# Kernel tuning notes

Hardware: AMD Instinct MI355X
Metric: run time of the kernel (lower is better)

The kernel has to match this reference:

```python
import jax, jax.numpy as jnp
import numpy as np

N, E = 100000, 1600000          # nodes, edges
H, DH = 8, 256                  # heads, dim_hidden
D = DH // H                     # dim per head
NEG_SLOPE = 0.2                 # GAT leaky_relu slope
BETA = 0.5


def setup_inputs() -> dict:
    key = jax.random.key(0)
    ks = jax.random.split(key, 10)
    s = 1.0 / np.sqrt(DH)
    return {
        "x": jax.random.normal(ks[0], (N, DH), jnp.float32),
        "edge_index": jax.random.randint(ks[1], (2, E), 0, N, jnp.int32),
        "edge_attr": jax.random.uniform(ks[2], (E,), jnp.float32),
        # GAT params (no bias, add_self_loops=False)
        "Wg": jax.random.normal(ks[3], (DH, DH), jnp.float32) * s,
        "att_src": jax.random.normal(ks[4], (H, D), jnp.float32) * s,
        "att_dst": jax.random.normal(ks[5], (H, D), jnp.float32) * s,
        # h_lin
        "Wh": jax.random.normal(ks[6], (DH, DH), jnp.float32) * s,
        "bh": jnp.zeros((DH,), jnp.float32),
        # lin
        "Wl": jax.random.normal(ks[7], (DH, DH), jnp.float32) * s,
        "bl": jnp.zeros((DH,), jnp.float32),
        # LayerNorm
        "ln_g": jnp.ones((DH,), jnp.float32),
        "ln_b": jnp.zeros((DH,), jnp.float32),
        # beta gate (beta>=0 -> constant vector)
        "b_param": jnp.full((DH,), BETA, jnp.float32),
    }


def _layer_norm(v, g, b, eps=1e-5):
    mu = jnp.mean(v, axis=-1, keepdims=True)
    var = jnp.var(v, axis=-1, keepdims=True)
    return (v - mu) * jax.lax.rsqrt(var + eps) * g + b


def _weighted_gat(x, edge_index, edge_attr, Wg, att_src, att_dst):
    # GATConv with per-edge weights folded into the softmax numerator.
    xs = (x @ Wg).reshape(N, H, D)                       # [N,H,D]
    a_src = jnp.einsum("nhd,hd->nh", xs, att_src)        # [N,H]
    a_dst = jnp.einsum("nhd,hd->nh", xs, att_dst)
    src, dst = edge_index[0], edge_index[1]
    e = jax.nn.leaky_relu(a_src[src] + a_dst[dst], NEG_SLOPE)   # [E,H]
    m = jax.ops.segment_max(e, dst, num_segments=N)             # [N,H]
    m = jnp.where(jnp.isfinite(m), m, 0.0)                      # isolated nodes
    p = jnp.exp(e - m[dst]) * edge_attr[:, None]                # weighted exp
    denom = jax.ops.segment_sum(p, dst, num_segments=N)         # [N,H]
    alpha = p / (denom[dst] + 1e-16)                            # [E,H]
    msg = alpha[:, :, None] * xs[src]                           # [E,H,D]
    out = jax.ops.segment_sum(msg, dst, num_segments=N)         # [N,H,D]
    return out.reshape(N, DH)


def reference(x, edge_index, edge_attr, Wg, att_src, att_dst, Wh, bh, Wl, bl, ln_g, ln_b, b_param):
    x_in = x
    h = jax.nn.relu(x @ Wh + bh)
    xg = _weighted_gat(x, edge_index, edge_attr, Wg, att_src, att_dst) + (x @ Wl + bl)
    xg = jax.nn.relu(xg)                                  # dropout p=0 (eval)
    beta = b_param[None, :]
    out = (1.0 - beta) * _layer_norm(h * xg, ln_g, ln_b) + beta * xg
    return out + x_in                                     # residual=True
```

## Files before the change

### kernel.cpp

```cpp
#include <hip/hip_runtime.h>

typedef __attribute__((ext_vector_type(4))) float f32x4;
typedef __attribute__((ext_vector_type(8))) __bf16 bf16x8;

__device__ __forceinline__ unsigned short f2bf(float f) {
    return __builtin_bit_cast(unsigned short, (__bf16)f);
}
__device__ __forceinline__ float bf2f(unsigned short u) {
    return __builtin_bit_cast(float, (unsigned)u << 16);
}

__device__ __forceinline__ void gload16(const void* g, void* l) {
    __builtin_amdgcn_global_load_lds(
        (const __attribute__((address_space(1))) void*)g,
        (__attribute__((address_space(3))) void*)l, 16, 0, 0);
}

__global__ __launch_bounds__(256) void k_prep(
    const float* __restrict__ x, unsigned short* __restrict__ xb, long total, long totalPad,
    const float* __restrict__ Wg, const float* __restrict__ Wh, const float* __restrict__ Wl,
    unsigned short* __restrict__ wt,
    const int* __restrict__ dst, int E, int* __restrict__ deg,
    int nCvt, int nHist) {
    const int b = blockIdx.x;
    const int tid = threadIdx.x;
    if (b < nCvt) {
        long i = ((long)b * 256 + tid) * 4;
        if (i >= totalPad) return;
        if (i < total) {
            float4 v = *(const float4*)(x + i);
            ushort4 u;
            u.x = f2bf(v.x); u.y = f2bf(v.y); u.z = f2bf(v.z); u.w = f2bf(v.w);
            *(ushort4*)(xb + i) = u;
        } else {
            ushort4 u = {0, 0, 0, 0};
            *(ushort4*)(xb + i) = u;
        }
    } else if (b < nCvt + 768) {
        int t = (b - nCvt) * 256 + tid;
        int nn = t >> 8, k = t & 255;
        const float* W = (nn < 256) ? Wg : (nn < 512) ? Wh : Wl;
        wt[t] = f2bf(W[k * 256 + (nn & 255)]);
    } else {
        int bb = b - nCvt - 768;
        for (int e = bb * 256 + tid; e < E; e += nHist * 256)
            atomicAdd(&deg[dst[e]], 1);
    }
}

__global__ __launch_bounds__(256, 4) void k_gemm(
    const unsigned short* __restrict__ A,
    const unsigned short* __restrict__ BT,
    unsigned short* __restrict__ xs, unsigned short* __restrict__ hb,
    unsigned short* __restrict__ xlb,
    const float* __restrict__ bh, const float* __restrict__ bl, int M, int nwg) {
    __shared__ char Asm[32768];
    const int bid = blockIdx.x;
    const int xcd = bid & 7, idx = bid >> 3;
    const int q = nwg >> 3, r = nwg & 7;
    const int tm = (xcd < r ? xcd * (q + 1) : r * (q + 1) + (xcd - r) * q) + idx;

    const int tid = threadIdx.x;
    const int lane = tid & 63;
    const int wave = tid >> 6;
    const int wn = wave * 32;
    const int fr = lane & 15;
    const int ko = (lane >> 4) * 8;

#pragma unroll
    for (int s = 0; s < 8; ++s) {
        const int c = s * 256 + tid;
        const int rr = c & 15;
        const int kc = (c >> 4) & 31;
        const int m16 = c >> 9;
        const unsigned short* g = A + (size_t)(tm * 64 + m16 * 16 + rr) * 256 + kc * 8;
        gload16(g, Asm + (size_t)c * 16);
    }
    __syncthreads();

    const char* Ab = Asm + lane * 16;

    for (int tn = 0; tn < 6; ++tn) {
        f32x4 acc[4][2] = {};
        const unsigned short* Bg = BT + (size_t)(tn * 128 + wn + fr) * 256 + ko;
#pragma unroll
        for (int ks = 0; ks < 8; ++ks) {
            bf16x8 bfr[2], af[4];
#pragma unroll
            for (int j = 0; j < 2; ++j)
                bfr[j] = *(const bf16x8*)(Bg + (size_t)j * 16 * 256 + ks * 32);
#pragma unroll
            for (int i = 0; i < 4; ++i)
                af[i] = *(const bf16x8*)(Ab + i * 8192 + ks * 1024);
#pragma unroll
            for (int i = 0; i < 4; ++i)
#pragma unroll
                for (int j = 0; j < 2; ++j)
                    acc[i][j] = __builtin_amdgcn_mfma_f32_16x16x32_bf16(af[i], bfr[j], acc[i][j], 0, 0, 0);
        }
        const int ob = tn >> 1;
        unsigned short* obuf = (ob == 0) ? xs : (ob == 1) ? hb : xlb;
        const float* bias = (ob == 1) ? bh : bl;
        const int rbase = tm * 64 + (lane >> 4) * 4;
#pragma unroll
        for (int i = 0; i < 4; ++i) {
#pragma unroll
            for (int j = 0; j < 2; ++j) {
                const int c0 = (tn & 1) * 128 + wn + j * 16 + fr;
                float bv = (ob == 0) ? 0.f : bias[c0];
#pragma unroll
                for (int q2 = 0; q2 < 4; ++q2) {
                    const int rg = rbase + i * 16 + q2;
                    if (rg < M) {
                        float v = acc[i][j][q2] + bv;
                        if (ob == 1) v = v > 0.f ? v : 0.f;
                        obuf[(size_t)rg * 256 + c0] = f2bf(v);
                    }
                }
            }
        }
    }
}

__global__ __launch_bounds__(256) void k_attn(const unsigned short* __restrict__ xs,
                                              const float* __restrict__ att_src,
                                              const float* __restrict__ att_dst,
                                              float* __restrict__ a_src,
                                              float* __restrict__ a_dst, int N) {
    int t = blockIdx.x * 256 + threadIdx.x;
    int n = t >> 3, hh = t & 7;
    if (n >= N) return;
    const ushort4* xp = (const ushort4*)(xs + (size_t)n * 256 + hh * 32);
    const float4* sp = (const float4*)(att_src + hh * 32);
    const float4* dp = (const float4*)(att_dst + hh * 32);
    float sa = 0.f, sd = 0.f;
#pragma unroll
    for (int q = 0; q < 8; ++q) {
        ushort4 u = xp[q];
        float4 s = sp[q], d = dp[q];
        float v0 = bf2f(u.x), v1 = bf2f(u.y), v2 = bf2f(u.z), v3 = bf2f(u.w);
        sa += v0 * s.x + v1 * s.y + v2 * s.z + v3 * s.w;
        sd += v0 * d.x + v1 * d.y + v2 * d.z + v3 * d.w;
    }
    a_src[t] = sa;
    a_dst[t] = sd;
}

__global__ __launch_bounds__(256) void k_scan1(const int* __restrict__ deg, int* __restrict__ offs,
                                               int* __restrict__ bsum, int Npad) {
    __shared__ int s[256];
    int t = threadIdx.x;
    int i = blockIdx.x * 256 + t;
    int v = (i < Npad) ? ((deg[i] + 7) & ~7) : 0;
    s[t] = v;
    __syncthreads();
#pragma unroll
    for (int off = 1; off < 256; off <<= 1) {
        int x = (t >= off) ? s[t - off] : 0;
        __syncthreads();
        s[t] += x;
        __syncthreads();
    }
    offs[i] = s[t] - v;
    if (t == 255) bsum[blockIdx.x] = s[255];
}

__global__ __launch_bounds__(512) void k_scan2(int* __restrict__ bsum, int nb) {
    __shared__ int s[512];
    int t = threadIdx.x;
    int v = (t < nb) ? bsum[t] : 0;
    s[t] = v;
    __syncthreads();
#pragma unroll
    for (int off = 1; off < 512; off <<= 1) {
        int x = (t >= off) ? s[t - off] : 0;
        __syncthreads();
        s[t] += x;
        __syncthreads();
    }
    if (t < nb) bsum[t] = s[t] - v;
}

__global__ __launch_bounds__(256) void k_scan3(int* __restrict__ offs, const int* __restrict__ bsum,
                                               int* __restrict__ cursor) {
    int i = blockIdx.x * 256 + threadIdx.x;
    int o = offs[i] + bsum[blockIdx.x];
    offs[i] = o;
    cursor[i] = o;
}

__global__ void k_edge(const int* __restrict__ ei, const float* __restrict__ ea, int E,
                       const float* __restrict__ a_src, const float* __restrict__ a_dst,
                       int* __restrict__ cursor, int* __restrict__ srcArr,
                       unsigned short* __restrict__ pvArr) {
    for (int e = blockIdx.x * blockDim.x + threadIdx.x; e < E; e += gridDim.x * blockDim.x) {
        const int s = ei[e];
        const int d = ei[(size_t)E + e];
        const float w = ea[e];
        const int pos = atomicAdd(&cursor[d], 1);
        const float4* As = (const float4*)(a_src + (size_t)s * 8);
        const float4* Ad = (const float4*)(a_dst + (size_t)d * 8);
        float4 s0 = As[0], s1 = As[1], d0 = Ad[0], d1 = Ad[1];
        float a[8] = {s0.x + d0.x, s0.y + d0.y, s0.z + d0.z, s0.w + d0.w,
                      s1.x + d1.x, s1.y + d1.y, s1.z + d1.z, s1.w + d1.w};
        unsigned pk[4];
#pragma unroll
        for (int h = 0; h < 4; ++h) {
            float lo = a[2 * h], hi = a[2 * h + 1];
            lo = (lo > 0.f) ? lo : 0.2f * lo;
            hi = (hi > 0.f) ? hi : 0.2f * hi;
            unsigned short plo = f2bf(__expf(lo) * w);
            unsigned short phi = f2bf(__expf(hi) * w);
            pk[h] = (unsigned)plo | ((unsigned)phi << 16);
        }
        srcArr[pos] = s;
        uint4 v = {pk[0], pk[1], pk[2], pk[3]};
        *(uint4*)(pvArr + (size_t)pos * 8) = v;
    }
}

__global__ __launch_bounds__(256) void k_agg(
    const int* __restrict__ offs, const int* __restrict__ deg,
    const int* __restrict__ srcArr, const unsigned short* __restrict__ pvArr,
    const unsigned short* __restrict__ xs, const unsigned short* __restrict__ hb,
    const unsigned short* __restrict__ xlb,
    const unsigned short* __restrict__ xbf, const float* __restrict__ ln_g,
    const float* __restrict__ ln_b,
    const float* __restrict__ beta, float* __restrict__ out, int N) {
    const int wave = threadIdx.x >> 6, lane = threadIdx.x & 63;
    const int n = blockIdx.x * 4 + wave;
    if (n >= N) return;
    const int start = offs[n];
    const int dpad = (deg[n] + 7) & ~7;
    const int head = lane >> 3;
    const int eSub = lane & 7;

    f32x4 acc = {0.f, 0.f, 0.f, 0.f};
    float dsum = 0.f;

    const int* sp = srcArr + start;
    const unsigned short* pp = pvArr + (size_t)start * 8 + head;
    const char* xsb = (const char*)xs;
    const unsigned rowoff = (unsigned)lane * 8;

    for (int g = 0; g < dpad; g += 8) {
        const int sA = sp[g + eSub];
        ushort4 rows[8];
        float pvv[8];
#pragma unroll
        for (int e = 0; e < 8; ++e)
            rows[e] = *(const ushort4*)(xsb + (size_t)(unsigned)__shfl(sA, e) * 512 + rowoff);
#pragma unroll
        for (int e = 0; e < 8; ++e)
            pvv[e] = bf2f(pp[(size_t)(g + e) * 8]);
#pragma unroll
        for (int e = 0; e < 8; ++e) {
            const float p = pvv[e];
            dsum += p;
            acc[0] += p * bf2f(rows[e].x);
            acc[1] += p * bf2f(rows[e].y);
            acc[2] += p * bf2f(rows[e].z);
            acc[3] += p * bf2f(rows[e].w);
        }
    }
    const float inv = 1.f / (dsum + 1e-16f);

    const size_t base = (size_t)n * 256 + lane * 4;
    ushort4 xlu = *(const ushort4*)(xlb + base);
    ushort4 hu = *(const ushort4*)(hb + base);
    ushort4 xiu = *(const ushort4*)(xbf + base);
    f32x4 xg, t4;
    float s1 = 0.f, s2 = 0.f;
    const float xl0[4] = {bf2f(xlu.x), bf2f(xlu.y), bf2f(xlu.z), bf2f(xlu.w)};
    const float hv0[4] = {bf2f(hu.x), bf2f(hu.y), bf2f(hu.z), bf2f(hu.w)};
    const float xi0[4] = {bf2f(xiu.x), bf2f(xiu.y), bf2f(xiu.z), bf2f(xiu.w)};
#pragma unroll
    for (int q = 0; q < 4; ++q) {
        float gg = acc[q] * inv + xl0[q];
        gg = gg > 0.f ? gg : 0.f;
        xg[q] = gg;
        float t = hv0[q] * gg;
        t4[q] = t;
        s1 += t;
        s2 += t * t;
    }
#pragma unroll
    for (int off = 32; off; off >>= 1) {
        s1 += __shfl_xor(s1, off);
        s2 += __shfl_xor(s2, off);
    }
    const float mu = s1 * (1.f / 256.f);
    const float var = s2 * (1.f / 256.f) - mu * mu;
    const float rs = rsqrtf(var + 1e-5f);

    f32x4 g4 = *(const f32x4*)(ln_g + lane * 4);
    f32x4 b4 = *(const f32x4*)(ln_b + lane * 4);
    f32x4 be = *(const f32x4*)(beta + lane * 4);
    f32x4 o;
#pragma unroll
    for (int q = 0; q < 4; ++q) {
        float ln = (t4[q] - mu) * rs * g4[q] + b4[q];
        o[q] = (1.f - be[q]) * ln + be[q] * xg[q] + xi0[q];
    }
    *(f32x4*)(out + base) = o;
}

extern "C" void kernel_launch(void* const* d_in, const int* in_sizes, int n_in,
                              void* d_out, int out_size, void* d_ws, size_t ws_size,
                              hipStream_t stream) {
    const float* x = (const float*)d_in[0];
    const int* ei = (const int*)d_in[1];
    const float* ea = (const float*)d_in[2];
    const float* Wg = (const float*)d_in[3];
    const float* att_src = (const float*)d_in[4];
    const float* att_dst = (const float*)d_in[5];
    const float* Wh = (const float*)d_in[6];
    const float* bh = (const float*)d_in[7];
    const float* Wl = (const float*)d_in[8];
    const float* bl = (const float*)d_in[9];
    const float* ln_g = (const float*)d_in[10];
    const float* ln_b = (const float*)d_in[11];
    const float* beta = (const float*)d_in[12];
    float* out = (float*)d_out;

    const int DH = 256;
    const int N = in_sizes[0] / DH;
    const int E = in_sizes[2];
    const int Mpad = ((N + 127) / 128) * 128;
    const int Npad = ((N + 255) / 256) * 256;
    const int nscanb = Npad / 256;
    const int nwg = Mpad / 64;
    const int nCvt = Mpad / 4;
    const int nHist = 2048;
    const size_t Epad = (size_t)E + 8 * (size_t)N;

    char* w = (char*)d_ws;
    auto take = [&](size_t bytes) -> char* {
        char* p = w;
        w += (bytes + 255) & ~(size_t)255;
        return p;
    };
    unsigned short* xs = (unsigned short*)take((size_t)N * DH * 2);
    unsigned short* hb = (unsigned short*)take((size_t)N * DH * 2);
    unsigned short* xlb = (unsigned short*)take((size_t)N * DH * 2);
    float* a_src = (float*)take((size_t)N * 8 * 4);
    float* a_dst = (float*)take((size_t)N * 8 * 4);
    unsigned short* xbf = (unsigned short*)take((size_t)Mpad * DH * 2);
    unsigned short* wt = (unsigned short*)take((size_t)768 * 256 * 2);
    int* deg = (int*)take((size_t)Npad * 4);
    int* offs = (int*)take((size_t)Npad * 4);
    int* cursor = (int*)take((size_t)Npad * 4);
    int* bsum = (int*)take(512 * 4);
    int* srcArr = (int*)take(Epad * 4);
    unsigned short* pvArr = (unsigned short*)take(Epad * 8 * 2);

    hipMemsetAsync(deg, 0, (size_t)Npad * 4, stream);
    hipMemsetAsync(srcArr, 0, Epad * 4, stream);
    hipMemsetAsync(pvArr, 0, Epad * 8 * 2, stream);

    k_prep<<<nCvt + 768 + nHist, 256, 0, stream>>>(x, xbf, (long)N * DH, (long)Mpad * DH,
                                                   Wg, Wh, Wl, wt, ei + E, E, deg, nCvt, nHist);

    k_scan1<<<nscanb, 256, 0, stream>>>(deg, offs, bsum, Npad);
    k_scan2<<<1, 512, 0, stream>>>(bsum, nscanb);
    k_scan3<<<nscanb, 256, 0, stream>>>(offs, bsum, cursor);

    k_gemm<<<nwg, 256, 0, stream>>>(xbf, wt, xs, hb, xlb, bh, bl, N, nwg);

    k_attn<<<(N * 8 + 255) / 256, 256, 0, stream>>>(xs, att_src, att_dst, a_src, a_dst, N);

    k_edge<<<2048, 256, 0, stream>>>(ei, ea, E, a_src, a_dst, cursor, srcArr, pvArr);

    k_agg<<<(N + 3) / 4, 256, 0, stream>>>(offs, deg, srcArr, pvArr,
                                           xs, hb, xlb, xbf, ln_g, ln_b, beta, out, N);
}
```

Measured before the change: 700.3 us.

## Restructure GEMM to keep weight tile in LDS and stream pre-tiled activation blocks

The prep kernel now writes x in bf16 already in the MFMA tile-cell layout, and the three weight matrices pre-transposed into the same cell layout. The GEMM becomes a grid of (row-block × 12 column tiles of 64). Each workgroup loads its 64-column weight slice into LDS once, then loops over 16 consecutive 64-row A tiles with a 2×2 wave split. This replaces per-iteration global B reads and makes A loads fully contiguous. The residual in the aggregation kernel now reads the original fp32 x instead of the bf16 copy. In exchange, each A tile is now reloaded by 12 workgroups, and the A-tile reload is serialized behind barriers.

```diff
diff --git a/kernel.cpp b/kernel.cpp
--- a/kernel.cpp
+++ b/kernel.cpp
@@ -17,97 +17,116 @@
 }
 
 __global__ __launch_bounds__(256) void k_prep(
-    const float* __restrict__ x, unsigned short* __restrict__ xb, long total, long totalPad,
+    const float* __restrict__ x, unsigned short* __restrict__ xA, int N,
     const float* __restrict__ Wg, const float* __restrict__ Wh, const float* __restrict__ Wl,
-    unsigned short* __restrict__ wt,
+    unsigned short* __restrict__ wtc,
     const int* __restrict__ dst, int E, int* __restrict__ deg,
-    int nCvt, int nHist) {
+    int nACell, int nWtc, int nHist) {
     const int b = blockIdx.x;
     const int tid = threadIdx.x;
-    if (b < nCvt) {
-        long i = ((long)b * 256 + tid) * 4;
-        if (i >= totalPad) return;
-        if (i < total) {
-            float4 v = *(const float4*)(x + i);
-            ushort4 u;
-            u.x = f2bf(v.x); u.y = f2bf(v.y); u.z = f2bf(v.z); u.w = f2bf(v.w);
-            *(ushort4*)(xb + i) = u;
-        } else {
-            ushort4 u = {0, 0, 0, 0};
-            *(ushort4*)(xb + i) = u;
-        }
-    } else if (b < nCvt + 768) {
-        int t = (b - nCvt) * 256 + tid;
-        int nn = t >> 8, k = t & 255;
-        const float* W = (nn < 256) ? Wg : (nn < 512) ? Wh : Wl;
-        wt[t] = f2bf(W[k * 256 + (nn & 255)]);
+    if (b < nACell) {
+#pragma unroll
+        for (int u = 0; u < 2; ++u) {
+            const long ci = ((long)b * 256 + tid) * 2 + u;
+            const int rt = (int)(ci >> 11);
+            const int c = (int)(ci & 2047);
+            const int m16 = c >> 9, kc = (c >> 4) & 31, rr = c & 15;
+            const int row = rt * 64 + m16 * 16 + rr;
+            ushort4 o0 = {0, 0, 0, 0}, o1 = {0, 0, 0, 0};
+            if (row < N) {
+                const float4* p = (const float4*)(x + (size_t)row * 256 + kc * 8);
+                float4 v0 = p[0], v1 = p[1];
+                o0.x = f2bf(v0.x); o0.y = f2bf(v0.y); o0.z = f2bf(v0.z); o0.w = f2bf(v0.w);
+                o1.x = f2bf(v1.x); o1.y = f2bf(v1.y); o1.z = f2bf(v1.z); o1.w = f2bf(v1.w);
+            }
+            *(ushort4*)(xA + ci * 8) = o0;
+            *(ushort4*)(xA + ci * 8 + 4) = o1;
+        }
+    } else if (b < nACell + nWtc) {
+        const int gi = (b - nACell) * 256 + tid;
+        const int tn2 = gi >> 11;
+        const int c = gi & 2047;
+        const int cg = c >> 9, kc = (c >> 4) & 31, cr = c & 15;
+        const int colg = tn2 * 64 + cg * 16 + cr;
+        const float* W = (colg < 256) ? Wg : (colg < 512) ? Wh : Wl;
+        const int c2 = colg & 255;
+        ushort4 o0, o1;
+        o0.x = f2bf(W[(kc * 8 + 0) * 256 + c2]);
+        o0.y = f2bf(W[(kc * 8 + 1) * 256 + c2]);
+        o0.z = f2bf(W[(kc * 8 + 2) * 256 + c2]);
+        o0.w = f2bf(W[(kc * 8 + 3) * 256 + c2]);
+        o1.x = f2bf(W[(kc * 8 + 4) * 256 + c2]);
+        o1.y = f2bf(W[(kc * 8 + 5) * 256 + c2]);
+        o1.z = f2bf(W[(kc * 8 + 6) * 256 + c2]);
+        o1.w = f2bf(W[(kc * 8 + 7) * 256 + c2]);
+        *(ushort4*)(wtc + (size_t)gi * 8) = o0;
+        *(ushort4*)(wtc + (size_t)gi * 8 + 4) = o1;
     } else {
-        int bb = b - nCvt - 768;
+        const int bb = b - nACell - nWtc;
         for (int e = bb * 256 + tid; e < E; e += nHist * 256)
             atomicAdd(&deg[dst[e]], 1);
     }
 }
 
-__global__ __launch_bounds__(256, 4) void k_gemm(
-    const unsigned short* __restrict__ A,
-    const unsigned short* __restrict__ BT,
+__global__ __launch_bounds__(256) void k_gemm(
+    const unsigned short* __restrict__ xA, const unsigned short* __restrict__ wtc,
     unsigned short* __restrict__ xs, unsigned short* __restrict__ hb,
     unsigned short* __restrict__ xlb,
-    const float* __restrict__ bh, const float* __restrict__ bl, int M, int nwg) {
+    const float* __restrict__ bh, const float* __restrict__ bl, int M, int NIT) {
     __shared__ char Asm[32768];
-    const int bid = blockIdx.x;
-    const int xcd = bid & 7, idx = bid >> 3;
-    const int q = nwg >> 3, r = nwg & 7;
-    const int tm = (xcd < r ? xcd * (q + 1) : r * (q + 1) + (xcd - r) * q) + idx;
-
+    __shared__ char Bsm[32768];
+    const int tn2 = blockIdx.x % 12;
+    const int tmb = blockIdx.x / 12;
     const int tid = threadIdx.x;
     const int lane = tid & 63;
     const int wave = tid >> 6;
-    const int wn = wave * 32;
+    const int wr = wave >> 1;
+    const int wc = wave & 1;
     const int fr = lane & 15;
-    const int ko = (lane >> 4) * 8;
-
-#pragma unroll
-    for (int s = 0; s < 8; ++s) {
-        const int c = s * 256 + tid;
-        const int rr = c & 15;
-        const int kc = (c >> 4) & 31;
-        const int m16 = c >> 9;
-        const unsigned short* g = A + (size_t)(tm * 64 + m16 * 16 + rr) * 256 + kc * 8;
-        gload16(g, Asm + (size_t)c * 16);
-    }
+
+    const long rt0 = (long)tmb * NIT;
+#pragma unroll
+    for (int s = 0; s < 8; ++s)
+        gload16(wtc + ((size_t)tn2 * 2048 + s * 256 + tid) * 8, Bsm + (s * 256 + tid) * 16);
+#pragma unroll
+    for (int s = 0; s < 8; ++s)
+        gload16(xA + (rt0 * 2048 + s * 256 + tid) * 8, Asm + (s * 256 + tid) * 16);
     __syncthreads();
 
-    const char* Ab = Asm + lane * 16;
-
-    for (int tn = 0; tn < 6; ++tn) {
-        f32x4 acc[4][2] = {};
-        const unsigned short* Bg = BT + (size_t)(tn * 128 + wn + fr) * 256 + ko;
+    const int ob = tn2 >> 2;
+    unsigned short* obuf = (ob == 0) ? xs : (ob == 1) ? hb : xlb;
+    const float* bias = (ob == 1) ? bh : bl;
+    const char* Ab = Asm + (wr * 2) * 8192 + lane * 16;
+    const char* Bb = Bsm + (wc * 2) * 8192 + lane * 16;
+
+    for (int it = 0; it < NIT; ++it) {
+        f32x4 acc[2][2] = {};
 #pragma unroll
         for (int ks = 0; ks < 8; ++ks) {
-            bf16x8 bfr[2], af[4];
-#pragma unroll
-            for (int j = 0; j < 2; ++j)
-                bfr[j] = *(const bf16x8*)(Bg + (size_t)j * 16 * 256 + ks * 32);
-#pragma unroll
-            for (int i = 0; i < 4; ++i)
-                af[i] = *(const bf16x8*)(Ab + i * 8192 + ks * 1024);
-#pragma unroll
-            for (int i = 0; i < 4; ++i)
-#pragma unroll
-                for (int j = 0; j < 2; ++j)
-                    acc[i][j] = __builtin_amdgcn_mfma_f32_16x16x32_bf16(af[i], bfr[j], acc[i][j], 0, 0, 0);
-        }
-        const int ob = tn >> 1;
-        unsigned short* obuf = (ob == 0) ? xs : (ob == 1) ? hb : xlb;
-        const float* bias = (ob == 1) ? bh : bl;
-        const int rbase = tm * 64 + (lane >> 4) * 4;
-#pragma unroll
-        for (int i = 0; i < 4; ++i) {
+            bf16x8 af[2], bb2[2];
+            af[0] = *(const bf16x8*)(Ab + ks * 1024);
+            af[1] = *(const bf16x8*)(Ab + 8192 + ks * 1024);
+            bb2[0] = *(const bf16x8*)(Bb + ks * 1024);
+            bb2[1] = *(const bf16x8*)(Bb + 8192 + ks * 1024);
+            acc[0][0] = __builtin_amdgcn_mfma_f32_16x16x32_bf16(af[0], bb2[0], acc[0][0], 0, 0, 0);
+            acc[0][1] = __builtin_amdgcn_mfma_f32_16x16x32_bf16(af[0], bb2[1], acc[0][1], 0, 0, 0);
+            acc[1][0] = __builtin_amdgcn_mfma_f32_16x16x32_bf16(af[1], bb2[0], acc[1][0], 0, 0, 0);
+            acc[1][1] = __builtin_amdgcn_mfma_f32_16x16x32_bf16(af[1], bb2[1], acc[1][1], 0, 0, 0);
+        }
+        __syncthreads();
+        if (it + 1 < NIT) {
+            const long rt = rt0 + it + 1;
+#pragma unroll
+            for (int s = 0; s < 8; ++s)
+                gload16(xA + (rt * 2048 + s * 256 + tid) * 8, Asm + (s * 256 + tid) * 16);
+        }
+        const int rbase = (int)((rt0 + it) * 64) + wr * 32 + (lane >> 4) * 4;
+#pragma unroll
+        for (int i = 0; i < 2; ++i) {
 #pragma unroll
             for (int j = 0; j < 2; ++j) {
-                const int c0 = (tn & 1) * 128 + wn + j * 16 + fr;
-                float bv = (ob == 0) ? 0.f : bias[c0];
+                const int c0 = (tn2 & 3) * 64 + wc * 32 + j * 16 + fr;
+                const float bv = (ob == 0) ? 0.f : bias[c0];
 #pragma unroll
                 for (int q2 = 0; q2 < 4; ++q2) {
                     const int rg = rbase + i * 16 + q2;
@@ -119,6 +138,7 @@
                 }
             }
         }
+        __syncthreads();
     }
 }
 
@@ -224,7 +244,7 @@
     const int* __restrict__ srcArr, const unsigned short* __restrict__ pvArr,
     const unsigned short* __restrict__ xs, const unsigned short* __restrict__ hb,
     const unsigned short* __restrict__ xlb,
-    const unsigned short* __restrict__ xbf, const float* __restrict__ ln_g,
+    const float* __restrict__ x, const float* __restrict__ ln_g,
     const float* __restrict__ ln_b,
     const float* __restrict__ beta, float* __restrict__ out, int N) {
     const int wave = threadIdx.x >> 6, lane = threadIdx.x & 63;
@@ -268,12 +288,10 @@
     const size_t base = (size_t)n * 256 + lane * 4;
     ushort4 xlu = *(const ushort4*)(xlb + base);
     ushort4 hu = *(const ushort4*)(hb + base);
-    ushort4 xiu = *(const ushort4*)(xbf + base);
     f32x4 xg, t4;
     float s1 = 0.f, s2 = 0.f;
     const float xl0[4] = {bf2f(xlu.x), bf2f(xlu.y), bf2f(xlu.z), bf2f(xlu.w)};
     const float hv0[4] = {bf2f(hu.x), bf2f(hu.y), bf2f(hu.z), bf2f(hu.w)};
-    const float xi0[4] = {bf2f(xiu.x), bf2f(xiu.y), bf2f(xiu.z), bf2f(xiu.w)};
 #pragma unroll
     for (int q = 0; q < 4; ++q) {
         float gg = acc[q] * inv + xl0[q];
@@ -296,11 +314,12 @@
     f32x4 g4 = *(const f32x4*)(ln_g + lane * 4);
     f32x4 b4 = *(const f32x4*)(ln_b + lane * 4);
     f32x4 be = *(const f32x4*)(beta + lane * 4);
+    f32x4 xin = *(const f32x4*)(x + base);
     f32x4 o;
 #pragma unroll
     for (int q = 0; q < 4; ++q) {
         float ln = (t4[q] - mu) * rs * g4[q] + b4[q];
-        o[q] = (1.f - be[q]) * ln + be[q] * xg[q] + xi0[q];
+        o[q] = (1.f - be[q]) * ln + be[q] * xg[q] + xin[q];
     }
     *(f32x4*)(out + base) = o;
 }
@@ -326,11 +345,14 @@
     const int DH = 256;
     const int N = in_sizes[0] / DH;
     const int E = in_sizes[2];
-    const int Mpad = ((N + 127) / 128) * 128;
+    const int NIT = 16;
+    const int nT0 = (N + 63) / 64;
+    const int nTiles = ((nT0 + NIT - 1) / NIT) * NIT;
+    const int RB = nTiles / NIT;
     const int Npad = ((N + 255) / 256) * 256;
     const int nscanb = Npad / 256;
-    const int nwg = Mpad / 64;
-    const int nCvt = Mpad / 4;
+    const int nACell = nTiles * 2048 / 512;
+    const int nWtc = 96;
     const int nHist = 2048;
     const size_t Epad = (size_t)E + 8 * (size_t)N;
 
@@ -345,8 +367,8 @@
     unsigned short* xlb = (unsigned short*)take((size_t)N * DH * 2);
     float* a_src = (float*)take((size_t)N * 8 * 4);
     float* a_dst = (float*)take((size_t)N * 8 * 4);
-    unsigned short* xbf = (unsigned short*)take((size_t)Mpad * DH * 2);
-    unsigned short* wt = (unsigned short*)take((size_t)768 * 256 * 2);
+    unsigned short* xA = (unsigned short*)take((size_t)nTiles * 32768);
+    unsigned short* wtc = (unsigned short*)take((size_t)24576 * 16);
     int* deg = (int*)take((size_t)Npad * 4);
     int* offs = (int*)take((size_t)Npad * 4);
     int* cursor = (int*)take((size_t)Npad * 4);
@@ -358,19 +380,19 @@
     hipMemsetAsync(srcArr, 0, Epad * 4, stream);
     hipMemsetAsync(pvArr, 0, Epad * 8 * 2, stream);
 
-    k_prep<<<nCvt + 768 + nHist, 256, 0, stream>>>(x, xbf, (long)N * DH, (long)Mpad * DH,
-                                                   Wg, Wh, Wl, wt, ei + E, E, deg, nCvt, nHist);
+    k_prep<<<nACell + nWtc + nHist, 256, 0, stream>>>(x, xA, N, Wg, Wh, Wl, wtc,
+                                                      ei + E, E, deg, nACell, nWtc, nHist);
 
     k_scan1<<<nscanb, 256, 0, stream>>>(deg, offs, bsum, Npad);
     k_scan2<<<1, 512, 0, stream>>>(bsum, nscanb);
     k_scan3<<<nscanb, 256, 0, stream>>>(offs, bsum, cursor);
 
-    k_gemm<<<nwg, 256, 0, stream>>>(xbf, wt, xs, hb, xlb, bh, bl, N, nwg);
+    k_gemm<<<RB * 12, 256, 0, stream>>>(xA, wtc, xs, hb, xlb, bh, bl, N, NIT);
 
     k_attn<<<(N * 8 + 255) / 256, 256, 0, stream>>>(xs, att_src, att_dst, a_src, a_dst, N);
 
     k_edge<<<2048, 256, 0, stream>>>(ei, ea, E, a_src, a_dst, cursor, srcArr, pvArr);
 
     k_agg<<<(N + 3) / 4, 256, 0, stream>>>(offs, deg, srcArr, pvArr,
-                                           xs, hb, xlb, xbf, ln_g, ln_b, beta, out, N);
-}
+                                           xs, hb, xlb, x, ln_g, ln_b, beta, out, N);
+}
```

Measured after the change: 601.5 us. 1.16x faster.
